# Kernel optimization log

Hardware: AMD Instinct MI355X
Metric: run time of the kernel (lower is better)

## Reference

```python
import jax, jax.numpy as jnp
import numpy as np

B, Q, K, D, H = 8, 1024, 1024, 1024, 16
HD = D // H
FFN = 4 * D


def layer_norm(x, w, b, eps=1e-5):
    mu = jnp.mean(x, axis=-1, keepdims=True)
    var = jnp.var(x, axis=-1, keepdims=True)
    return (x - mu) * jax.lax.rsqrt(var + eps) * w + b


def setup_inputs() -> dict:
    key = jax.random.key(0)
    ks = jax.random.split(key, 10)
    query = jax.random.normal(ks[0], (B, Q, D), dtype=jnp.float32)
    key_value = jax.random.normal(ks[1], (B, K, D), dtype=jnp.float32)
    kpm = jax.random.randint(ks[2], (B, K), 0, 2).astype(bool)
    kpm = kpm.at[:, 0].set(True)  # guarantee >=1 valid key per row
    s = 0.02
    return {
        "query": query,
        "key_value": key_value,
        "key_padding_mask": kpm,
        "ln_q_w": jnp.ones((D,), jnp.float32), "ln_q_b": jnp.zeros((D,), jnp.float32),
        "ln_kv_w": jnp.ones((D,), jnp.float32), "ln_kv_b": jnp.zeros((D,), jnp.float32),
        "ln_f_w": jnp.ones((D,), jnp.float32), "ln_f_b": jnp.zeros((D,), jnp.float32),
        "in_proj_w": jax.random.normal(ks[3], (3 * D, D), jnp.float32) * s,
        "in_proj_b": jnp.zeros((3 * D,), jnp.float32),
        "out_proj_w": jax.random.normal(ks[4], (D, D), jnp.float32) * s,
        "out_proj_b": jnp.zeros((D,), jnp.float32),
        "ffn_w1": jax.random.normal(ks[5], (FFN, D), jnp.float32) * s,
        "ffn_b1": jnp.zeros((FFN,), jnp.float32),
        "ffn_w2": jax.random.normal(ks[6], (D, FFN), jnp.float32) * s,
        "ffn_b2": jnp.zeros((D,), jnp.float32),
    }


def reference(query, key_value, key_padding_mask,
              ln_q_w, ln_q_b, ln_kv_w, ln_kv_b, ln_f_w, ln_f_b,
              in_proj_w, in_proj_b, out_proj_w, out_proj_b,
              ffn_w1, ffn_b1, ffn_w2, ffn_b2):
    q_norm = layer_norm(query, ln_q_w, ln_q_b)
    kv_norm = layer_norm(key_value, ln_kv_w, ln_kv_b)

    Wq, Wk, Wv = jnp.split(in_proj_w, 3, axis=0)
    bq, bk, bv = jnp.split(in_proj_b, 3, axis=0)
    q = (q_norm @ Wq.T + bq).reshape(B, Q, H, HD).transpose(0, 2, 1, 3)  # (B,H,Q,hd)
    k = (kv_norm @ Wk.T + bk).reshape(B, K, H, HD).transpose(0, 2, 1, 3)
    v = (kv_norm @ Wv.T + bv).reshape(B, K, H, HD).transpose(0, 2, 1, 3)

    scale = 1.0 / jnp.sqrt(jnp.float32(HD))
    scores = jnp.einsum('bhqd,bhkd->bhqk', q * scale, k)  # (B,H,Q,K)
    scores = jnp.where(key_padding_mask[:, None, None, :], scores, -jnp.inf)
    attn = jax.nn.softmax(scores, axis=-1)

    attn_out = jnp.einsum('bhqk,bhkd->bhqd', attn, v)
    attn_out = attn_out.transpose(0, 2, 1, 3).reshape(B, Q, D)
    attn_out = attn_out @ out_proj_w.T + out_proj_b

    x = query + attn_out
    h = layer_norm(x, ln_f_w, ln_f_b)
    h = jax.nn.gelu(h @ ffn_w1.T + ffn_b1, approximate=False)
    x = x + (h @ ffn_w2.T + ffn_b2)

    attn_weights = jnp.mean(attn, axis=1)  # average over heads -> (B,Q,K)
    return x, attn_weights
```

## Files before the change

kernel.cpp:

```cpp
#include <hip/hip_runtime.h>
#include <math.h>

typedef short  s16x8 __attribute__((ext_vector_type(8)));
typedef short  s16x4 __attribute__((ext_vector_type(4)));
typedef float  f32x4 __attribute__((ext_vector_type(4)));

#define DEV static __device__ __forceinline__
#define M0SHIFT 3.0f
#define LOG2E   1.44269504088896f
#define SCL2F   0.18033688011112f

#if __has_builtin(__builtin_amdgcn_exp2f)
#define EXP2F(x) __builtin_amdgcn_exp2f(x)
#else
#define EXP2F(x) exp2f(x)
#endif

DEV float b2f(unsigned short h) {
    unsigned int u = ((unsigned int)h) << 16;
    float f; __builtin_memcpy(&f, &u, 4); return f;
}
DEV unsigned short f2b(float f) {
    unsigned int u; __builtin_memcpy(&u, &f, 4);
    unsigned int r = (u + 0x7fffu + ((u >> 16) & 1u)) >> 16;
    return (unsigned short)r;
}
DEV unsigned fb(float x) { unsigned u; __builtin_memcpy(&u, &x, 4); return u; }
DEV s16x4 pack4(float a0, float a1, float a2, float a3) {
    unsigned lo = __builtin_amdgcn_perm(fb(a1), fb(a0), 0x07060302u);
    unsigned hi = __builtin_amdgcn_perm(fb(a3), fb(a2), 0x07060302u);
    unsigned long long p = ((unsigned long long)hi << 32) | lo;
    s16x4 r; __builtin_memcpy(&r, &p, 8); return r;
}

#define GLD16(gp, lp) __builtin_amdgcn_global_load_lds( \
    (const __attribute__((address_space(1))) unsigned int*)(const void*)(gp), \
    (__attribute__((address_space(3))) unsigned int*)(void*)(lp), 16, 0, 0)

#if __has_builtin(__builtin_amdgcn_mfma_f32_16x16x16_bf16)
#define MFMA16(a, b, c) __builtin_amdgcn_mfma_f32_16x16x16_bf16(a, b, c, 0, 0, 0)
#else
#define MFMA16(a, b, c) __builtin_amdgcn_mfma_f32_16x16x16bf16_1k(a, b, c, 0, 0, 0)
#endif

DEV float ldsel(const void* p, size_t i, bool f32) {
    return f32 ? ((const float*)p)[i] : b2f(((const unsigned short*)p)[i]);
}
DEV s16x8 ld8sel(const void* p, size_t eidx, bool f32) {
    if (f32) {
        const float* f = (const float*)p + eidx;
        f32x4 a = *(const f32x4*)f;
        f32x4 b = *(const f32x4*)(f + 4);
        s16x8 o;
        o[0]=(short)f2b(a[0]); o[1]=(short)f2b(a[1]); o[2]=(short)f2b(a[2]); o[3]=(short)f2b(a[3]);
        o[4]=(short)f2b(b[0]); o[5]=(short)f2b(b[1]); o[6]=(short)f2b(b[2]); o[7]=(short)f2b(b[3]);
        return o;
    }
    return *(const s16x8*)((const unsigned short*)p + eidx);
}

__global__ __launch_bounds__(256) void dtype_probe(
    const unsigned int* __restrict__ q, int* __restrict__ flag)
{
    int t = threadIdx.x;
    int hits = 0;
    for (int i = t; i < 2048; i += 256) {
        unsigned e0 = (q[i] >> 7) & 0xFFu;
        hits += (e0 >= 0x70u && e0 <= 0x87u) ? 1 : 0;
    }
#pragma unroll
    for (int m = 32; m >= 1; m >>= 1) hits += __shfl_xor(hits, m);
    __shared__ int sh[4];
    if ((t & 63) == 0) sh[t >> 6] = hits;
    __syncthreads();
    if (t == 0) *flag = (sh[0] + sh[1] + sh[2] + sh[3] > 1024) ? 0 : 1;
}

__global__ __launch_bounds__(1024) void mask_prep(
    const unsigned int* __restrict__ w, const unsigned char* __restrict__ bytes,
    float* __restrict__ mf)
{
    __shared__ int flag;
    const int t = threadIdx.x;
    if (t == 0) flag = 0;
    __syncthreads();
    unsigned int a = w[t], b = w[t + 1024];
    if (a > 1u || b > 1u) flag = 1;
    __syncthreads();
    const int f = flag;
    const float NEGINF = -__builtin_inff();
#pragma unroll
    for (int i = 0; i < 8; i++) {
        int c = t * 8 + i;
        int v = f ? (int)(bytes[c] != 0) : (int)(w[c] != 0);
        mf[c] = v ? (-M0SHIFT * LOG2E) : NEGINF;
    }
}

struct CvtArgs { const void* s[8]; };
__global__ __launch_bounds__(256) void cvt_w(
    const int* __restrict__ flagp, CvtArgs a, unsigned short* __restrict__ dst)
{
    const int f = *flagp;
    size_t e = ((size_t)blockIdx.x * 256 + threadIdx.x) * 8;
    if (e >= 12592128u) return;
    const size_t off[9] = {0u, 3145728u, 4194304u, 8388608u, 12582912u,
                           12585984u, 12587008u, 12591104u, 12592128u};
    int s = 0;
    while (e >= off[s + 1]) s++;
    *(s16x8*)&dst[e] = ld8sel(a.s[s], e - off[s], f == 1);
}

__global__ __launch_bounds__(256) void ln_k(
    const int* __restrict__ flagp, int xmode, int wmode,
    const void* __restrict__ x1p, const void* __restrict__ w1p, const void* __restrict__ b1p,
    unsigned short* __restrict__ y1p,
    const void* __restrict__ x2p, const void* __restrict__ w2p, const void* __restrict__ b2p,
    unsigned short* __restrict__ y2p)
{
    const int f = *flagp;
    const bool xf = (xmode == 2) ? (f == 1) : (xmode == 1);
    const bool wf = (wmode == 2) ? (f == 1) : (wmode == 1);
    int row = blockIdx.x;
    const void* x = x1p; const void* wgt = w1p; const void* bias = b1p;
    unsigned short* y = y1p;
    if (x2p && row >= 8192) {
        row -= 8192; x = x2p; wgt = w2p; bias = b2p; y = y2p;
    }
    const int t = threadIdx.x;
    const int w = t >> 6, lane = t & 63;
    float f0, f1, f2, f3;
    if (xf) {
        f32x4 v = *(const f32x4*)((const float*)x + (size_t)row * 1024 + t * 4);
        f0 = v[0]; f1 = v[1]; f2 = v[2]; f3 = v[3];
    } else {
        s16x4 v = *(const s16x4*)((const unsigned short*)x + (size_t)row * 1024 + t * 4);
        f0 = b2f((unsigned short)v[0]); f1 = b2f((unsigned short)v[1]);
        f2 = b2f((unsigned short)v[2]); f3 = b2f((unsigned short)v[3]);
    }
    __shared__ float red[4];
    float s = f0 + f1 + f2 + f3;
#pragma unroll
    for (int m = 32; m >= 1; m >>= 1) s += __shfl_xor(s, m);
    if (lane == 0) red[w] = s;
    __syncthreads();
    float mu = (red[0] + red[1] + red[2] + red[3]) * (1.0f / 1024.0f);
    float d0 = f0 - mu, d1 = f1 - mu, d2 = f2 - mu, d3 = f3 - mu;
    float q = d0 * d0 + d1 * d1 + d2 * d2 + d3 * d3;
#pragma unroll
    for (int m = 32; m >= 1; m >>= 1) q += __shfl_xor(q, m);
    __syncthreads();
    if (lane == 0) red[w] = q;
    __syncthreads();
    float var = (red[0] + red[1] + red[2] + red[3]) * (1.0f / 1024.0f);
    float rs = rsqrtf(var + 1e-5f);
    s16x4 vo;
    vo[0] = (short)f2b(d0 * rs * ldsel(wgt, t*4+0, wf) + ldsel(bias, t*4+0, wf));
    vo[1] = (short)f2b(d1 * rs * ldsel(wgt, t*4+1, wf) + ldsel(bias, t*4+1, wf));
    vo[2] = (short)f2b(d2 * rs * ldsel(wgt, t*4+2, wf) + ldsel(bias, t*4+2, wf));
    vo[3] = (short)f2b(d3 * rs * ldsel(wgt, t*4+3, wf) + ldsel(bias, t*4+3, wf));
    *(s16x4*)&y[(size_t)row * 1024 + t * 4] = vo;
}

__global__ __launch_bounds__(256) void gemm_bt(
    const int* __restrict__ flagp,
    const unsigned short* __restrict__ A,
    const void* __restrict__ W, size_t woff, int wmode,
    const void* __restrict__ bias, size_t boff, int bmode,
    const void* __restrict__ res, int rmode,
    void* __restrict__ C, int omode,
    int M, int N, int Kd, int ldw, int ldc, int act)
{
    const int f = *flagp;
    const bool wf = (wmode == 2) && (f == 1);
    __shared__ alignas(16) unsigned short As[128 * 32];
    __shared__ alignas(16) unsigned short Bs[128 * 32];
    const int t = threadIdx.x;
    const int m0 = blockIdx.y * 128, n0 = blockIdx.x * 128;
    const int w = t >> 6, lane = t & 63, quad = lane >> 4, l16 = lane & 15;
    const int wm = (w >> 1) * 64, wn = (w & 1) * 64;
    const f32x4 zero = {0.f, 0.f, 0.f, 0.f};
    f32x4 acc[4][4];
#pragma unroll
    for (int i = 0; i < 4; i++)
#pragma unroll
        for (int j = 0; j < 4; j++) acc[i][j] = zero;
    const int r0 = t >> 2, c0 = (t & 3) * 8;
    unsigned short* AsW = As + (size_t)w * 512;
    unsigned short* BsW = Bs + (size_t)w * 512;
    const unsigned short* W16 = (const unsigned short*)W + woff;
    const float*          W32 = (const float*)W + woff;

    for (int kt = 0; kt < Kd; kt += 32) {
        GLD16(&A[(size_t)(m0 + r0) * Kd + kt + c0],      AsW);
        GLD16(&A[(size_t)(m0 + r0 + 64) * Kd + kt + c0], AsW + 2048);
        if (wf) {
            *(s16x8*)&Bs[r0 * 32 + c0]        = ld8sel(W32, (size_t)(n0 + r0) * ldw + kt + c0, true);
            *(s16x8*)&Bs[(r0 + 64) * 32 + c0] = ld8sel(W32, (size_t)(n0 + r0 + 64) * ldw + kt + c0, true);
        } else {
            GLD16(&W16[(size_t)(n0 + r0) * ldw + kt + c0],      BsW);
            GLD16(&W16[(size_t)(n0 + r0 + 64) * ldw + kt + c0], BsW + 2048);
        }
        __syncthreads();
        s16x8 af[4], bfr[4];
#pragma unroll
        for (int i = 0; i < 4; i++) {
            af[i]  = *(const s16x8*)&As[(wm + i * 16 + l16) * 32 + quad * 8];
            bfr[i] = *(const s16x8*)&Bs[(wn + i * 16 + l16) * 32 + quad * 8];
        }
#pragma unroll
        for (int mi = 0; mi < 4; mi++)
#pragma unroll
            for (int ni = 0; ni < 4; ni++)
                acc[mi][ni] = __builtin_amdgcn_mfma_f32_16x16x32_bf16(af[mi], bfr[ni], acc[mi][ni], 0, 0, 0);
        __syncthreads();
    }
    const bool bf = (bmode == 2) && (f == 1);
    const bool rf = (rmode == 2) || (rmode == 3 && f == 1);
    const bool of = (omode == 1) || (omode == 2 && f == 1);
#pragma unroll
    for (int mi = 0; mi < 4; mi++)
#pragma unroll
        for (int ni = 0; ni < 4; ni++)
#pragma unroll
            for (int r = 0; r < 4; r++) {
                int gr = m0 + wm + mi * 16 + quad * 4 + r;
                int gc = n0 + wn + ni * 16 + l16;
                float v = acc[mi][ni][r];
                if (bmode >= 0) v += ldsel(bias, boff + gc, bf);
                if (act) v = 0.5f * v * (1.f + erff(v * 0.70710678118f));
                if (rmode) v += ldsel(res, (size_t)gr * ldc + gc, rf);
                size_t ci = (size_t)gr * ldc + gc;
                if (of) ((float*)C)[ci] = v;
                else ((unsigned short*)C)[ci] = f2b(v);
            }
}

__global__ __launch_bounds__(512, 2) void gemm8(
    const unsigned short* __restrict__ A,
    const unsigned short* __restrict__ W, size_t woff,
    const unsigned short* __restrict__ bias, size_t boff,
    unsigned short* __restrict__ C,
    int Kd, int ldc, int act)
{
    __shared__ alignas(16) unsigned short lds[65536];
    const unsigned short* Wp = W + woff;
    const int t = threadIdx.x;
    const int w = t >> 6, lane = t & 63, quad = lane >> 4, l16 = lane & 15;
    const int wr = w >> 2, wcn = w & 3;

    const int gx = (int)gridDim.x;
    const int nwg = gx * (int)gridDim.y;
    const int lid = (int)blockIdx.y * gx + (int)blockIdx.x;
    const int swz = (lid & 7) * (nwg >> 3) + (lid >> 3);
    const int m0 = (swz / gx) * 256, n0 = (swz % gx) * 256;

    const int hrow = w * 16 + (lane >> 3);
    const int scol = ((lane & 7) ^ ((lane & 32) ? 2 : 0)) * 8;
    const int NT = Kd >> 6;

    const int swq = (l16 & 4) ? 16 : 0;
    const int ck0 = (quad * 8) ^ swq;
    const int ck1 = (32 + quad * 8) ^ swq;

    const f32x4 zero = {0.f, 0.f, 0.f, 0.f};
    f32x4 acc[8][4];
#pragma unroll
    for (int i = 0; i < 8; i++)
#pragma unroll
        for (int j = 0; j < 4; j++) acc[i][j] = zero;
    s16x8 aF[4][2], bLo[2][2], bHi[2][2];

#define SA8(bb,h,tt,g) GLD16(&A[(size_t)(m0 + (h)*128 + hrow + (g)*8) * Kd + (size_t)(tt)*64 + scol], \
                             &lds[(bb)*32768 + (h)*8192 + (w*16 + (g)*8)*64])
#define SB8(bb,h,tt,g) GLD16(&Wp[(size_t)(n0 + (h)*128 + hrow + (g)*8) * Kd + (size_t)(tt)*64 + scol], \
                             &lds[(bb)*32768 + 16384 + (h)*8192 + (w*16 + (g)*8)*64])
#define LDA8(bb,q) { _Pragma("unroll") for (int i_ = 0; i_ < 4; i_++) { \
        const int ar_ = (q)*128 + wr*64 + i_*16 + l16; \
        aF[i_][0] = *(const s16x8*)&lds[(bb)*32768 + ar_*64 + ck0]; \
        aF[i_][1] = *(const s16x8*)&lds[(bb)*32768 + ar_*64 + ck1]; } }
#define LDB8(bb,dst,q) { _Pragma("unroll") for (int j_ = 0; j_ < 2; j_++) { \
        const int br_ = (q)*128 + wcn*32 + j_*16 + l16; \
        dst[j_][0] = *(const s16x8*)&lds[(bb)*32768 + 16384 + br_*64 + ck0]; \
        dst[j_][1] = *(const s16x8*)&lds[(bb)*32768 + 16384 + br_*64 + ck1]; } }
#define MM8(mq,nq,bsrc) { __builtin_amdgcn_s_setprio(1); \
        _Pragma("unroll") for (int i_ = 0; i_ < 4; i_++) \
        _Pragma("unroll") for (int j_ = 0; j_ < 2; j_++) { \
            acc[(mq)*4+i_][(nq)*2+j_] = __builtin_amdgcn_mfma_f32_16x16x32_bf16(aF[i_][0], bsrc[j_][0], acc[(mq)*4+i_][(nq)*2+j_], 0, 0, 0); \
            acc[(mq)*4+i_][(nq)*2+j_] = __builtin_amdgcn_mfma_f32_16x16x32_bf16(aF[i_][1], bsrc[j_][1], acc[(mq)*4+i_][(nq)*2+j_], 0, 0, 0); } \
        __builtin_amdgcn_s_setprio(0); }
#define BAR8() __builtin_amdgcn_s_barrier()
#define VMW8(n) asm volatile("s_waitcnt vmcnt(" #n ")" ::: "memory")

    SA8(0, 0, 0, 0); SA8(0, 0, 0, 1);
    SB8(0, 0, 0, 0); SB8(0, 0, 0, 1);
    SB8(0, 1, 0, 0); SB8(0, 1, 0, 1);
    SA8(0, 1, 0, 0); SA8(0, 1, 0, 1);
    VMW8(4); BAR8();

    for (int tt = 0; tt < NT - 1; tt++) {
        const int bb = tt & 1, nb = bb ^ 1;
        SA8(nb, 0, tt + 1, 0); SA8(nb, 0, tt + 1, 1);
        LDA8(bb, 0); LDB8(bb, bLo, 0);
        MM8(0, 0, bLo);
        VMW8(4); BAR8();
        SB8(nb, 0, tt + 1, 0); SB8(nb, 0, tt + 1, 1);
        LDB8(bb, bHi, 1);
        MM8(0, 1, bHi);
        VMW8(4); BAR8();
        SB8(nb, 1, tt + 1, 0); SB8(nb, 1, tt + 1, 1);
        LDA8(bb, 1);
        MM8(1, 1, bHi);
        BAR8();
        SA8(nb, 1, tt + 1, 0); SA8(nb, 1, tt + 1, 1);
        MM8(1, 0, bLo);
        VMW8(4); BAR8();
    }
    {
        const int bb = (NT - 1) & 1;
        LDA8(bb, 0); LDB8(bb, bLo, 0); MM8(0, 0, bLo); VMW8(2); BAR8();
        LDB8(bb, bHi, 1);              MM8(0, 1, bHi); VMW8(0); BAR8();
        LDA8(bb, 1);                   MM8(1, 1, bHi);
        MM8(1, 0, bLo);
    }

#pragma unroll
    for (int nq = 0; nq < 2; nq++)
#pragma unroll
    for (int j = 0; j < 2; j++) {
        const int gc = n0 + nq * 128 + wcn * 32 + j * 16 + l16;
        const float bv = b2f(bias[boff + gc]);
#pragma unroll
        for (int mq = 0; mq < 2; mq++)
#pragma unroll
        for (int i = 0; i < 4; i++)
#pragma unroll
        for (int r = 0; r < 4; r++) {
            const int gr = m0 + mq * 128 + wr * 64 + i * 16 + quad * 4 + r;
            float v = acc[mq * 4 + i][nq * 2 + j][r] + bv;
            if (act) v = 0.5f * v * (1.f + erff(v * 0.70710678118f));
            C[(size_t)gr * ldc + gc] = f2b(v);
        }
    }
#undef SA8
#undef SB8
#undef LDA8
#undef LDB8
#undef MM8
#undef BAR8
#undef VMW8
}

__global__ __launch_bounds__(512, 2) void gemm8n(
    const int* __restrict__ flagp,
    const unsigned short* __restrict__ A,
    const unsigned short* __restrict__ W, size_t woff, int ldw,
    const unsigned short* __restrict__ bias, size_t boff, int bmode,
    const void* __restrict__ res, int rmode,
    void* __restrict__ C, int omode,
    int Kd, int ldc)
{
    __shared__ alignas(16) unsigned short lds[49152];
    const int f = *flagp;
    const unsigned short* Wp = W + woff;
    const int t = threadIdx.x;
    const int w = t >> 6, lane = t & 63, quad = lane >> 4, l16 = lane & 15;
    const int wr = w >> 2, wcn = w & 3;

    const int gx = (int)gridDim.x;
    const int nwg = gx * (int)gridDim.y;
    const int lid = (int)blockIdx.y * gx + (int)blockIdx.x;
    const int swz = (lid & 7) * (nwg >> 3) + (lid >> 3);
    const int m0 = (swz / gx) * 256, n0 = (swz % gx) * 128;

    const int hrow = w * 16 + (lane >> 3);
    const int scol = ((lane & 7) ^ ((lane & 32) ? 2 : 0)) * 8;
    const int NT = Kd >> 6;

    const int swq = (l16 & 4) ? 16 : 0;
    const int ck0 = (quad * 8) ^ swq;
    const int ck1 = (32 + quad * 8) ^ swq;

    const f32x4 zero = {0.f, 0.f, 0.f, 0.f};
    f32x4 acc[8][2];
#pragma unroll
    for (int i = 0; i < 8; i++) { acc[i][0] = zero; acc[i][1] = zero; }
    s16x8 aF[4][2], bF[2][2];

#define SAN(bb,h,tt,g) GLD16(&A[(size_t)(m0 + (h)*128 + hrow + (g)*8) * Kd + (size_t)(tt)*64 + scol], \
                             &lds[(bb)*24576 + (h)*8192 + (w*16 + (g)*8)*64])
#define SBN(bb,tt,g)   GLD16(&Wp[(size_t)(n0 + hrow + (g)*8) * ldw + (size_t)(tt)*64 + scol], \
                             &lds[(bb)*24576 + 16384 + (w*16 + (g)*8)*64])
#define LDAN(bb,q) { _Pragma("unroll") for (int i_ = 0; i_ < 4; i_++) { \
        const int ar_ = wr*64 + i_*16 + l16; \
        aF[i_][0] = *(const s16x8*)&lds[(bb)*24576 + (q)*8192 + ar_*64 + ck0]; \
        aF[i_][1] = *(const s16x8*)&lds[(bb)*24576 + (q)*8192 + ar_*64 + ck1]; } }
#define LDBN(bb) { _Pragma("unroll") for (int j_ = 0; j_ < 2; j_++) { \
        const int br_ = wcn*32 + j_*16 + l16; \
        bF[j_][0] = *(const s16x8*)&lds[(bb)*24576 + 16384 + br_*64 + ck0]; \
        bF[j_][1] = *(const s16x8*)&lds[(bb)*24576 + 16384 + br_*64 + ck1]; } }
#define MMN(mq) { __builtin_amdgcn_s_setprio(1); \
        _Pragma("unroll") for (int i_ = 0; i_ < 4; i_++) \
        _Pragma("unroll") for (int j_ = 0; j_ < 2; j_++) { \
            acc[(mq)*4+i_][j_] = __builtin_amdgcn_mfma_f32_16x16x32_bf16(aF[i_][0], bF[j_][0], acc[(mq)*4+i_][j_], 0, 0, 0); \
            acc[(mq)*4+i_][j_] = __builtin_amdgcn_mfma_f32_16x16x32_bf16(aF[i_][1], bF[j_][1], acc[(mq)*4+i_][j_], 0, 0, 0); } \
        __builtin_amdgcn_s_setprio(0); }
#define BARN() __builtin_amdgcn_s_barrier()
#define VMWN(n) asm volatile("s_waitcnt vmcnt(" #n ")" ::: "memory")

    SAN(0, 0, 0, 0); SAN(0, 0, 0, 1);
    SBN(0, 0, 0);    SBN(0, 0, 1);
    SAN(0, 1, 0, 0); SAN(0, 1, 0, 1);
    VMWN(2); BARN();

    for (int tt = 0; tt < NT - 1; tt++) {
        const int bb = tt & 1, nb = bb ^ 1;
        SAN(nb, 0, tt + 1, 0); SAN(nb, 0, tt + 1, 1);
        SBN(nb, tt + 1, 0);    SBN(nb, tt + 1, 1);
        LDAN(bb, 0); LDBN(bb);
        MMN(0);
        VMWN(4); BARN();
        SAN(nb, 1, tt + 1, 0); SAN(nb, 1, tt + 1, 1);
        LDAN(bb, 1);
        MMN(1);
        VMWN(2); BARN();
    }
    {
        const int bb = (NT - 1) & 1;
        LDAN(bb, 0); LDBN(bb); MMN(0); VMWN(0); BARN();
        LDAN(bb, 1);           MMN(1);
    }

    const bool rf = (rmode == 2) || (rmode == 3 && f == 1);
    const bool of = (omode == 1) || (omode == 2 && f == 1);
#pragma unroll
    for (int j = 0; j < 2; j++) {
        const int gc = n0 + wcn * 32 + j * 16 + l16;
        const float bv = (bmode >= 0) ? b2f(bias[boff + gc]) : 0.f;
#pragma unroll
        for (int mq = 0; mq < 2; mq++)
#pragma unroll
        for (int i = 0; i < 4; i++)
#pragma unroll
        for (int r = 0; r < 4; r++) {
            const int gr = m0 + mq * 128 + wr * 64 + i * 16 + quad * 4 + r;
            float v = acc[mq * 4 + i][j][r] + bv;
            if (rmode) v += ldsel(res, (size_t)gr * ldc + gc, rf);
            size_t ci = (size_t)gr * ldc + gc;
            if (of) ((float*)C)[ci] = v;
            else ((unsigned short*)C)[ci] = f2b(v);
        }
    }
#undef SAN
#undef SBN
#undef LDAN
#undef LDBN
#undef MMN
#undef BARN
#undef VMWN
}

__global__ __launch_bounds__(256) void repack_kv(
    const unsigned short* __restrict__ kvp,
    unsigned short* __restrict__ kf, unsigned short* __restrict__ vf)
{
    const bool isv = blockIdx.x >= 4096;
    int t = (blockIdx.x - (isv ? 4096 : 0)) * 256 + threadIdx.x;
    int lane = t & 63;
    int quad = lane >> 4, l16 = lane & 15;
    if (!isv) {
        int half = (t >> 6) & 1, tile = (t >> 7) & 63;
        int h = (t >> 13) & 15, b = t >> 17;
        s16x8 v = *(const s16x8*)&kvp[(size_t)(b * 1024 + tile * 16 + l16) * 2048
                                      + h * 64 + half * 32 + quad * 8];
        *(s16x8*)&kf[(size_t)t * 8] = v;
    } else {
        int dt = (t >> 6) & 3, kt5 = (t >> 8) & 31;
        int h = (t >> 13) & 15, b = t >> 17;
        int d = dt * 16 + l16;
        s16x8 o;
#pragma unroll
        for (int j = 0; j < 8; j++) {
            int k = kt5 * 32 + ((j < 4) ? (quad * 4 + j) : (16 + quad * 4 + j - 4));
            o[j] = (short)kvp[(size_t)(b * 1024 + k) * 2048 + 1024 + h * 64 + d];
        }
        *(s16x8*)&vf[(size_t)t * 8] = o;
    }
}

__global__ __launch_bounds__(256, 4) void flash_attn(
    const unsigned short* __restrict__ qp, const unsigned short* __restrict__ kf,
    const unsigned short* __restrict__ vf, const float* __restrict__ maskf,
    unsigned short* __restrict__ ao, float* __restrict__ ml)
{
    const int bh = blockIdx.x;
    const int b = bh >> 4, h = bh & 15;
    const int t = threadIdx.x, w = t >> 6, lane = t & 63, quad = lane >> 4, l16 = lane & 15;
    const int q0 = (blockIdx.y * 4 + w) * 32;
    const f32x4 zero = {0.f, 0.f, 0.f, 0.f};

    const unsigned short* kfb = kf + (size_t)bh * 65536;
    const unsigned short* vfb = vf + (size_t)bh * 65536;

    const size_t qbA = (size_t)(b * 1024 + q0 + l16) * 1024 + h * 64 + quad * 8;
    const size_t qbB = qbA + (size_t)16 * 1024;
    s16x8 qa0 = *(const s16x8*)&qp[qbA], qa1 = *(const s16x8*)&qp[qbA + 32];
    s16x8 qb0 = *(const s16x8*)&qp[qbB], qb1 = *(const s16x8*)&qp[qbB + 32];

    f32x4 OA[4], OB[4];
#pragma unroll
    for (int dt = 0; dt < 4; dt++) { OA[dt] = zero; OB[dt] = zero; }
    float lsA = 0.f, lsB = 0.f;

    for (int kt = 0; kt < 1024; kt += 32) {
        const int tile2 = (kt >> 4) * 2;
        s16x8 k00 = *(const s16x8*)&kfb[(size_t)(tile2 + 0) * 512 + lane * 8];
        s16x8 k01 = *(const s16x8*)&kfb[(size_t)(tile2 + 1) * 512 + lane * 8];
        s16x8 k10 = *(const s16x8*)&kfb[(size_t)(tile2 + 2) * 512 + lane * 8];
        s16x8 k11 = *(const s16x8*)&kfb[(size_t)(tile2 + 3) * 512 + lane * 8];
        const size_t vrow = (size_t)(kt >> 5) * 4;
        s16x8 vv[4];
#pragma unroll
        for (int dt = 0; dt < 4; dt++)
            vv[dt] = *(const s16x8*)&vfb[(vrow + dt) * 512 + lane * 8];

        f32x4 SA0 = __builtin_amdgcn_mfma_f32_16x16x32_bf16(k00, qa0, zero, 0, 0, 0);
        SA0 = __builtin_amdgcn_mfma_f32_16x16x32_bf16(k01, qa1, SA0, 0, 0, 0);
        f32x4 SA1 = __builtin_amdgcn_mfma_f32_16x16x32_bf16(k10, qa0, zero, 0, 0, 0);
        SA1 = __builtin_amdgcn_mfma_f32_16x16x32_bf16(k11, qa1, SA1, 0, 0, 0);
        f32x4 SB0 = __builtin_amdgcn_mfma_f32_16x16x32_bf16(k00, qb0, zero, 0, 0, 0);
        SB0 = __builtin_amdgcn_mfma_f32_16x16x32_bf16(k01, qb1, SB0, 0, 0, 0);
        f32x4 SB1 = __builtin_amdgcn_mfma_f32_16x16x32_bf16(k10, qb0, zero, 0, 0, 0);
        SB1 = __builtin_amdgcn_mfma_f32_16x16x32_bf16(k11, qb1, SB1, 0, 0, 0);

        f32x4 mk0 = *(const f32x4*)&maskf[b * 1024 + kt + quad * 4];
        f32x4 mk1 = *(const f32x4*)&maskf[b * 1024 + kt + 16 + quad * 4];
        float xA0[4], xA1[4], xB0[4], xB1[4];
#pragma unroll
        for (int r = 0; r < 4; r++) {
            xA0[r] = EXP2F(SA0[r] * SCL2F + mk0[r]);
            xA1[r] = EXP2F(SA1[r] * SCL2F + mk1[r]);
            xB0[r] = EXP2F(SB0[r] * SCL2F + mk0[r]);
            xB1[r] = EXP2F(SB1[r] * SCL2F + mk1[r]);
        }
        float rsA = (xA0[0] + xA0[1]) + (xA0[2] + xA0[3])
                  + (xA1[0] + xA1[1]) + (xA1[2] + xA1[3]);
        float rsB = (xB0[0] + xB0[1]) + (xB0[2] + xB0[3])
                  + (xB1[0] + xB1[1]) + (xB1[2] + xB1[3]);
        rsA += __shfl_xor(rsA, 16);  rsA += __shfl_xor(rsA, 32);
        rsB += __shfl_xor(rsB, 16);  rsB += __shfl_xor(rsB, 32);
        lsA += rsA;  lsB += rsB;

        s16x4 pA0 = pack4(xA0[0], xA0[1], xA0[2], xA0[3]);
        s16x4 pA1 = pack4(xA1[0], xA1[1], xA1[2], xA1[3]);
        s16x4 pB0 = pack4(xB0[0], xB0[1], xB0[2], xB0[3]);
        s16x4 pB1 = pack4(xB1[0], xB1[1], xB1[2], xB1[3]);
#pragma unroll
        for (int dt = 0; dt < 4; dt++) {
            s16x4 v0 = {vv[dt][0], vv[dt][1], vv[dt][2], vv[dt][3]};
            s16x4 v1 = {vv[dt][4], vv[dt][5], vv[dt][6], vv[dt][7]};
            OA[dt] = MFMA16(pA0, v0, OA[dt]);
            OA[dt] = MFMA16(pA1, v1, OA[dt]);
            OB[dt] = MFMA16(pB0, v0, OB[dt]);
            OB[dt] = MFMA16(pB1, v1, OB[dt]);
        }
    }
    float liA = (lsA > 0.f) ? 1.f / lsA : 0.f;
    float liB = (lsB > 0.f) ? 1.f / lsB : 0.f;
    float libA[4], libB[4];
#pragma unroll
    for (int r = 0; r < 4; r++) {
        libA[r] = __shfl(liA, quad * 4 + r);
        libB[r] = __shfl(liB, quad * 4 + r);
    }
#pragma unroll
    for (int dt = 0; dt < 4; dt++)
#pragma unroll
        for (int r = 0; r < 4; r++) {
            int qrA = q0 + quad * 4 + r;
            ao[(size_t)(b * 1024 + qrA) * 1024 + h * 64 + dt * 16 + l16] = f2b(OA[dt][r] * libA[r]);
            ao[(size_t)(b * 1024 + qrA + 16) * 1024 + h * 64 + dt * 16 + l16] = f2b(OB[dt][r] * libB[r]);
        }
    if (lane < 16) {
        size_t ix = ((size_t)(b * 16 + h) * 1024 + q0 + l16) * 2;
        ml[ix] = M0SHIFT;      ml[ix + 1] = lsA;
        ml[ix + 32] = M0SHIFT; ml[ix + 33] = lsB;
    }
}

__global__ __launch_bounds__(512, 1) void attn_mean_k(
    const int* __restrict__ flagp,
    const unsigned short* __restrict__ qp, const unsigned short* __restrict__ kf,
    const float* __restrict__ maskf, const float* __restrict__ ml,
    void* __restrict__ dout)
{
    __shared__ alignas(16) unsigned short klds[65536];
    const bool of = (*flagp == 1);
    const size_t SHIFT = (size_t)8 * 1024 * 1024;
    const int b = blockIdx.x, q0 = blockIdx.y * 16;
    const int t = threadIdx.x, w = t >> 6, lane = t & 63, quad = lane >> 4, l16 = lane & 15;
    const int kbase = w * 128;
    const float NEGINF = -__builtin_inff();
    const f32x4 zero = {0.f, 0.f, 0.f, 0.f};
    unsigned short* kw = klds + (size_t)w * 8192;
    f32x4 acc[8];
#pragma unroll
    for (int i = 0; i < 8; i++) acc[i] = zero;
    float mka[8];
#pragma unroll
    for (int i = 0; i < 8; i++)
        mka[i] = maskf[b * 1024 + kbase + i * 16 + l16];

    for (int h = 0; h < 16; h++) {
        const unsigned short* kfb = kf + ((size_t)(b * 16 + h) * 128 + (kbase >> 4) * 2) * 512;
#pragma unroll
        for (int g = 0; g < 16; g++)
            GLD16(&kfb[(size_t)g * 512 + lane * 8], &kw[g * 512]);
        const size_t qb = (size_t)(b * 1024 + q0 + l16) * 1024 + h * 64 + quad * 8;
        s16x8 a0 = *(const s16x8*)&qp[qb];
        s16x8 a1 = *(const s16x8*)&qp[qb + 32];
        float cex2[4];
#pragma unroll
        for (int r = 0; r < 4; r++) {
            size_t ix = ((size_t)(b * 16 + h) * 1024 + q0 + quad * 4 + r) * 2;
            float lv = ml[ix + 1];
            cex2[r] = (lv > 0.f) ? ((M0SHIFT - ml[ix]) * LOG2E - log2f(lv)) : NEGINF;
        }
        asm volatile("s_waitcnt vmcnt(0)" ::: "memory");
#pragma unroll
        for (int i = 0; i < 8; i++) {
            s16x8 k0 = *(const s16x8*)&kw[(i * 2 + 0) * 512 + lane * 8];
            s16x8 k1 = *(const s16x8*)&kw[(i * 2 + 1) * 512 + lane * 8];
            f32x4 S = __builtin_amdgcn_mfma_f32_16x16x32_bf16(a0, k0, zero, 0, 0, 0);
            S = __builtin_amdgcn_mfma_f32_16x16x32_bf16(a1, k1, S, 0, 0, 0);
#pragma unroll
            for (int r = 0; r < 4; r++)
                acc[i][r] += EXP2F(S[r] * SCL2F + (mka[i] + cex2[r]));
        }
        asm volatile("" ::: "memory");
    }
#pragma unroll
    for (int i = 0; i < 8; i++)
#pragma unroll
        for (int r = 0; r < 4; r++) {
            int qrow = q0 + quad * 4 + r;
            size_t oi = SHIFT + (size_t)(b * 1024 + qrow) * 1024 + kbase + i * 16 + l16;
            float v = acc[i][r] * 0.0625f;
            if (of) ((float*)dout)[oi] = v;
            else ((unsigned short*)dout)[oi] = f2b(v);
        }
}

extern "C" void kernel_launch(void* const* d_in, const int* in_sizes, int n_in,
                              void* d_out, int out_size, void* d_ws, size_t ws_size,
                              hipStream_t stream) {
    const void* query = d_in[0];
    const void* keyv  = d_in[1];
    const void* maskr = d_in[2];
    const void* lqw = d_in[3];  const void* lqb = d_in[4];
    const void* lkw = d_in[5];  const void* lkb = d_in[6];
    const void* lfw = d_in[7];  const void* lfb = d_in[8];
    const void* ipw = d_in[9];  const void* ipb = d_in[10];
    const void* opw = d_in[11]; const void* opb = d_in[12];
    const void* w1  = d_in[13]; const void* b1  = d_in[14];
    const void* w2  = d_in[15]; const void* b2  = d_in[16];

    char* ws = (char*)d_ws;
    const size_t MB = 1024 * 1024;
    unsigned short* qn  = (unsigned short*)(ws + 0 * MB);
    unsigned short* kvn = (unsigned short*)(ws + 16 * MB);
    unsigned short* qpj = (unsigned short*)(ws + 32 * MB);
    unsigned short* kvp = (unsigned short*)(ws + 48 * MB);
    unsigned short* kfr = (unsigned short*)(ws + 80 * MB);
    unsigned short* vfr = (unsigned short*)(ws + 16 * MB);
    float*          ml  = (float*)(ws + 96 * MB);
    int*            fl  = (int*)(ws + 97 * MB);
    float*          mf  = (float*)(ws + 97 * MB + 256 * 1024);
    unsigned short* aco = (unsigned short*)(ws + 0 * MB);
    float*          xbf = (float*)(ws + 16 * MB);
    unsigned short* hn  = (unsigned short*)(ws + 48 * MB);
    unsigned short* g   = (unsigned short*)(ws + 64 * MB);
    unsigned short* wc  = (unsigned short*)(ws + 98 * MB);

    const bool big = ws_size >= (size_t)125 * MB;
    const size_t cWq = 0, cWk = 1048576, cWo = 3145728;
    const size_t cW1 = 4194304, cW2 = 8388608;
    const size_t cBq = 12582912, cBo = 12585984, cB1 = 12587008, cB2 = 12591104;

    const void *Wq, *Wk, *Wo, *Wf1, *Wf2, *Bq, *Bo, *Bf1, *Bf2;
    size_t wq_o, wk_o, wo_o, w1_o, w2_o, bq_o, bk_o, bo_o, b1_o, b2_o;
    int wm, bm;
    if (big) {
        Wq = Wk = Wo = Wf1 = Wf2 = Bq = Bo = Bf1 = Bf2 = wc;
        wq_o = cWq; wk_o = cWk; wo_o = cWo; w1_o = cW1; w2_o = cW2;
        bq_o = cBq; bk_o = cBq + 1024; bo_o = cBo; b1_o = cB1; b2_o = cB2;
        wm = 0; bm = 0;
    } else {
        Wq = Wk = ipw; Wo = opw; Wf1 = w1; Wf2 = w2;
        Bq = ipb; Bo = opb; Bf1 = b1; Bf2 = b2;
        wq_o = 0; wk_o = 1048576; wo_o = 0; w1_o = 0; w2_o = 0;
        bq_o = 0; bk_o = 1024; bo_o = 0; b1_o = 0; b2_o = 0;
        wm = 2; bm = 2;
    }

    dtype_probe<<<1, 256, 0, stream>>>((const unsigned int*)query, fl);
    mask_prep<<<1, 1024, 0, stream>>>((const unsigned int*)maskr, (const unsigned char*)maskr, mf);
    if (big) {
        CvtArgs ca; ca.s[0] = ipw; ca.s[1] = opw; ca.s[2] = w1; ca.s[3] = w2;
        ca.s[4] = ipb; ca.s[5] = opb; ca.s[6] = b1; ca.s[7] = b2;
        cvt_w<<<6149, 256, 0, stream>>>(fl, ca, wc);
    }

    ln_k<<<16384, 256, 0, stream>>>(fl, 2, 2, query, lqw, lqb, qn, keyv, lkw, lkb, kvn);

    if (big) {
        gemm8n<<<dim3(8, 32), 512, 0, stream>>>(fl, qn, wc, cWq, 1024, wc, cBq, 0,
                                                nullptr, 0, qpj, 0, 1024, 1024);
        gemm8<<<dim3(8, 32), 512, 0, stream>>>(kvn, wc, wk_o, wc, bk_o,
                                               kvp, 1024, 2048, 0);
    } else {
        gemm_bt<<<dim3(8, 64), 256, 0, stream>>>(fl, qn,  Wq, wq_o, wm, Bq, bq_o, bm,
                                                 nullptr, 0, qpj, 0, 8192, 1024, 1024, 1024, 1024, 0);
        gemm_bt<<<dim3(16, 64), 256, 0, stream>>>(fl, kvn, Wk, wk_o, wm, Bq, bk_o, bm,
                                                  nullptr, 0, kvp, 0, 8192, 2048, 1024, 1024, 2048, 0);
    }

    repack_kv<<<8192, 256, 0, stream>>>(kvp, kfr, vfr);
    flash_attn<<<dim3(128, 8), 256, 0, stream>>>(qpj, kfr, vfr, mf, aco, ml);
    attn_mean_k<<<dim3(8, 64), 512, 0, stream>>>(fl, qpj, kfr, mf, ml, d_out);

    if (big) {
        gemm8n<<<dim3(8, 32), 512, 0, stream>>>(fl, aco, wc, cWo, 1024, wc, cBo, 0,
                                                query, 3, xbf, 1, 1024, 1024);
    } else {
        gemm_bt<<<dim3(8, 64), 256, 0, stream>>>(fl, aco, Wo, wo_o, wm, Bo, bo_o, bm,
                                                 query, 3, xbf, 1, 8192, 1024, 1024, 1024, 1024, 0);
    }
    ln_k<<<8192, 256, 0, stream>>>(fl, 1, 2, xbf, lfw, lfb, hn,
                                   nullptr, nullptr, nullptr, nullptr);

    if (big) {
        gemm8<<<dim3(8, 32), 512, 0, stream>>>(hn, wc, w1_o, wc, b1_o,
                                               g, 1024, 2048, 1);
        gemm8n<<<dim3(8, 32), 512, 0, stream>>>(fl, g, wc, cW2, 4096, wc, cB2, 0,
                                                xbf, 2, xbf, 1, 2048, 1024);
        gemm8<<<dim3(8, 32), 512, 0, stream>>>(hn, wc, w1_o + (size_t)2048 * 1024, wc, b1_o + 2048,
                                               g, 1024, 2048, 1);
        gemm8n<<<dim3(8, 32), 512, 0, stream>>>(fl, g, wc, cW2 + 2048, 4096, nullptr, 0, -1,
                                                xbf, 2, d_out, 2, 2048, 1024);
    } else {
        gemm_bt<<<dim3(16, 64), 256, 0, stream>>>(fl, hn, Wf1, w1_o, wm, Bf1, b1_o, bm,
                                                  nullptr, 0, g, 0, 8192, 2048, 1024, 1024, 2048, 1);
        gemm_bt<<<dim3(8, 64), 256, 0, stream>>>(fl, g, Wf2, w2_o, wm, Bf2, b2_o, bm,
                                                 xbf, 2, xbf, 1, 8192, 1024, 2048, 4096, 1024, 0);
        gemm_bt<<<dim3(16, 64), 256, 0, stream>>>(fl, hn, Wf1, w1_o + (size_t)2048 * 1024, wm,
                                                  Bf1, b1_o + 2048, bm,
                                                  nullptr, 0, g, 0, 8192, 2048, 1024, 1024, 2048, 1);
        gemm_bt<<<dim3(8, 64), 256, 0, stream>>>(fl, g, Wf2, w2_o + 2048, wm,
                                                 nullptr, 0, -1,
                                                 xbf, 2, d_out, 2, 8192, 1024, 2048, 4096, 1024, 0);
    }
}
```

Before: 721.3 us.

## Double-buffer K tile loads across heads in attention-weights kernel

Splits each wave's per-head K tile in LDS into two halves. The next head's halves are prefetched, along with its Q fragment and softmax stats, while the current head's halves are consumed by the MFMA and exp2 work. Partial vmcnt waits replace the old full drain before every head's compute, so global-to-LDS latency overlaps with math. This adds register pressure for the prefetched Q and stats, and correctness depends on exact vmcnt accounting.

```diff
diff --git a/kernel.cpp b/kernel.cpp
--- a/kernel.cpp
+++ b/kernel.cpp
@@ -611,34 +611,61 @@
     for (int i = 0; i < 8; i++)
         mka[i] = maskf[b * 1024 + kbase + i * 16 + l16];
 
+#define AMK_ISSUE(h, hf, bs) { _Pragma("unroll") for (int g_ = 0; g_ < 8; g_++) \
+        GLD16(&kf[((size_t)(b * 16 + (h)) * 128 + (kbase >> 4) * 2 + (hf) * 8 + g_) * 512 + lane * 8], \
+              &kw[(bs) * 4096 + g_ * 512]); }
+#define AMK_QLD(h, d0, d1) { \
+        const size_t qb_ = (size_t)(b * 1024 + q0 + l16) * 1024 + (h) * 64 + quad * 8; \
+        d0 = *(const s16x8*)&qp[qb_]; d1 = *(const s16x8*)&qp[qb_ + 32]; }
+#define AMK_CEX(h, dst) { _Pragma("unroll") for (int r_ = 0; r_ < 4; r_++) { \
+        size_t ix_ = ((size_t)(b * 16 + (h)) * 1024 + q0 + quad * 4 + r_) * 2; \
+        float lv_ = ml[ix_ + 1]; \
+        dst[r_] = (lv_ > 0.f) ? ((M0SHIFT - ml[ix_]) * LOG2E - log2f(lv_)) : NEGINF; } }
+#define AMK_COMP(hf, bs, c0a, c1a, cexv) { _Pragma("unroll") for (int j_ = 0; j_ < 4; j_++) { \
+        s16x8 k0_ = *(const s16x8*)&kw[(bs) * 4096 + (2 * j_) * 512 + lane * 8]; \
+        s16x8 k1_ = *(const s16x8*)&kw[(bs) * 4096 + (2 * j_ + 1) * 512 + lane * 8]; \
+        f32x4 S_ = __builtin_amdgcn_mfma_f32_16x16x32_bf16(c0a, k0_, zero, 0, 0, 0); \
+        S_ = __builtin_amdgcn_mfma_f32_16x16x32_bf16(c1a, k1_, S_, 0, 0, 0); \
+        _Pragma("unroll") for (int r_ = 0; r_ < 4; r_++) \
+            acc[(hf) * 4 + j_][r_] += EXP2F(S_[r_] * SCL2F + (mka[(hf) * 4 + j_] + cexv[r_])); } }
+#define AMK_VMW8() asm volatile("s_waitcnt vmcnt(8)" ::: "memory")
+#define AMK_VMW0() asm volatile("s_waitcnt vmcnt(0)" ::: "memory")
+#define AMK_LGKM() asm volatile("s_waitcnt lgkmcnt(0)" ::: "memory")
+
+    s16x8 a0, a1, a0n, a1n;
+    float cex[4], cexn[4];
+    AMK_QLD(0, a0, a1);
+    AMK_CEX(0, cex);
+    AMK_ISSUE(0, 0, 0);
+    AMK_ISSUE(0, 1, 1);
+
     for (int h = 0; h < 16; h++) {
-        const unsigned short* kfb = kf + ((size_t)(b * 16 + h) * 128 + (kbase >> 4) * 2) * 512;
-#pragma unroll
-        for (int g = 0; g < 16; g++)
-            GLD16(&kfb[(size_t)g * 512 + lane * 8], &kw[g * 512]);
-        const size_t qb = (size_t)(b * 1024 + q0 + l16) * 1024 + h * 64 + quad * 8;
-        s16x8 a0 = *(const s16x8*)&qp[qb];
-        s16x8 a1 = *(const s16x8*)&qp[qb + 32];
-        float cex2[4];
-#pragma unroll
-        for (int r = 0; r < 4; r++) {
-            size_t ix = ((size_t)(b * 16 + h) * 1024 + q0 + quad * 4 + r) * 2;
-            float lv = ml[ix + 1];
-            cex2[r] = (lv > 0.f) ? ((M0SHIFT - ml[ix]) * LOG2E - log2f(lv)) : NEGINF;
-        }
-        asm volatile("s_waitcnt vmcnt(0)" ::: "memory");
-#pragma unroll
-        for (int i = 0; i < 8; i++) {
-            s16x8 k0 = *(const s16x8*)&kw[(i * 2 + 0) * 512 + lane * 8];
-            s16x8 k1 = *(const s16x8*)&kw[(i * 2 + 1) * 512 + lane * 8];
-            f32x4 S = __builtin_amdgcn_mfma_f32_16x16x32_bf16(a0, k0, zero, 0, 0, 0);
-            S = __builtin_amdgcn_mfma_f32_16x16x32_bf16(a1, k1, S, 0, 0, 0);
-#pragma unroll
-            for (int r = 0; r < 4; r++)
-                acc[i][r] += EXP2F(S[r] * SCL2F + (mka[i] + cex2[r]));
-        }
-        asm volatile("" ::: "memory");
-    }
+        AMK_VMW8();
+        AMK_COMP(0, 0, a0, a1, cex);
+        AMK_LGKM();
+        if (h < 15) {
+            AMK_QLD(h + 1, a0n, a1n);
+            AMK_CEX(h + 1, cexn);
+            AMK_ISSUE(h + 1, 0, 0);
+        }
+        if (h < 15) { AMK_VMW8(); } else { AMK_VMW0(); }
+        AMK_COMP(1, 1, a0, a1, cex);
+        AMK_LGKM();
+        if (h < 15) {
+            AMK_ISSUE(h + 1, 1, 1);
+            a0 = a0n; a1 = a1n;
+#pragma unroll
+            for (int r = 0; r < 4; r++) cex[r] = cexn[r];
+        }
+    }
+#undef AMK_ISSUE
+#undef AMK_QLD
+#undef AMK_CEX
+#undef AMK_COMP
+#undef AMK_VMW8
+#undef AMK_VMW0
+#undef AMK_LGKM
+
 #pragma unroll
     for (int i = 0; i < 8; i++)
 #pragma unroll
```

After: 721.9 us. No clear change (+0.1%).
